# Kernel optimization log

Measured on AMD Instinct MI355X. Metric: run time of the kernel, lower is better.

The kernel has to match this reference:

```python
import jax, jax.numpy as jnp
import numpy as np
from jax import lax

B = 128; LEADS = 12; T = 1000; DM = 128; DI = 256; DS = 16; DR = 8; DC = 4; NB = 4; L = 199; OUT = 256


def _ln(x, g, b):
    m = x.mean(-1, keepdims=True)
    v = ((x - m) ** 2).mean(-1, keepdims=True)
    return (x - m) * lax.rsqrt(v + 1e-5) * g + b


def _ssm_scan(u, delta, A, Bm, Cm, D):
    """Selective scan. u, delta: [B,L,DI]; Bm, Cm: [B,L,DS]; A: [DI,DS]; D: [DI]."""
    def step(h, inp):
        d_t, B_t, C_t, u_t = inp  # [B,DI],[B,DS],[B,DS],[B,DI]
        dA = jnp.exp(d_t[:, :, None] * A[None])            # [B,DI,DS]
        h = dA * h + (d_t * u_t)[:, :, None] * B_t[:, None, :]
        y = jnp.einsum('bds,bs->bd', h, C_t)
        return h, y
    h0 = jnp.zeros((u.shape[0], A.shape[0], A.shape[1]), u.dtype)
    xs = (jnp.moveaxis(delta, 1, 0), jnp.moveaxis(Bm, 1, 0),
          jnp.moveaxis(Cm, 1, 0), jnp.moveaxis(u, 1, 0))
    _, ys = lax.scan(step, h0, xs)
    return jnp.moveaxis(ys, 0, 1) + u * D[None, None, :]


def setup_inputs() -> dict:
    key = jax.random.key(0)
    ks = jax.random.split(key, 16)
    n = lambda k, shp, s: jax.random.normal(k, shp, jnp.float32) * s
    inp = {}
    inp['x'] = jax.random.normal(ks[0], (B, LEADS, T), jnp.float32)
    inp['pe_w'] = n(ks[1], (DM, LEADS, 10), 0.1)
    inp['pe_b'] = jnp.zeros((DM,), jnp.float32)
    inp['gn_g'] = jnp.ones((DM,), jnp.float32)
    inp['gn_b'] = jnp.zeros((DM,), jnp.float32)
    inp['pos'] = n(ks[2], (1, L, DM), 0.02)
    inp['ln1_g'] = jnp.ones((NB, DM), jnp.float32)
    inp['ln1_b'] = jnp.zeros((NB, DM), jnp.float32)
    inp['in_w'] = n(ks[3], (NB, 2 * DI, DM), 0.05)
    inp['conv_w'] = n(ks[4], (NB, DI, DC), 0.2)
    inp['conv_b'] = jnp.zeros((NB, DI), jnp.float32)
    inp['xproj_w'] = n(ks[5], (NB, DR + 2 * DS, DI), 0.05)
    inp['dtproj_w'] = n(ks[6], (NB, DI, DR), 0.2)
    inp['dtproj_b'] = jnp.full((NB, DI), -4.6, jnp.float32)  # softplus(-4.6) ~= 0.01
    inp['A_log'] = jnp.tile(jnp.log(jnp.arange(1, DS + 1, dtype=jnp.float32))[None, None, :], (NB, DI, 1))
    inp['Dp'] = jnp.ones((NB, DI), jnp.float32)
    inp['outw'] = n(ks[7], (NB, DM, DI), 0.05)
    inp['ln2_g'] = jnp.ones((NB, DM), jnp.float32)
    inp['ln2_b'] = jnp.zeros((NB, DM), jnp.float32)
    inp['ffn_w1'] = n(ks[8], (NB, 4 * DM, DM), 0.05)
    inp['ffn_b1'] = jnp.zeros((NB, 4 * DM), jnp.float32)
    inp['ffn_w2'] = n(ks[9], (NB, DM, 4 * DM), 0.05)
    inp['ffn_b2'] = jnp.zeros((NB, DM), jnp.float32)
    inp['lnf_g'] = jnp.ones((DM,), jnp.float32)
    inp['lnf_b'] = jnp.zeros((DM,), jnp.float32)
    inp['head_w'] = n(ks[10], (OUT, DM), 0.05)
    inp['head_b'] = jnp.zeros((OUT,), jnp.float32)
    return inp


def reference(x, pe_w, pe_b, gn_g, gn_b, pos, ln1_g, ln1_b, in_w, conv_w, conv_b,
              xproj_w, dtproj_w, dtproj_b, A_log, Dp, outw, ln2_g, ln2_b,
              ffn_w1, ffn_b1, ffn_w2, ffn_b2, lnf_g, lnf_b, head_w, head_b):
    # --- patch embed: Conv1d(12 -> DM, k=10, s=5) + GroupNorm(8) + GELU ---
    h = lax.conv_general_dilated(x, pe_w, (5,), 'VALID',
                                 dimension_numbers=('NCH', 'OIH', 'NCH'))
    h = h + pe_b[None, :, None]                      # [B, DM, L]
    Bb, _, Lc = h.shape
    hg = h.reshape(Bb, 8, DM // 8, Lc)
    m = hg.mean((2, 3), keepdims=True)
    v = ((hg - m) ** 2).mean((2, 3), keepdims=True)
    h = ((hg - m) * lax.rsqrt(v + 1e-5)).reshape(Bb, DM, Lc)
    h = h * gn_g[None, :, None] + gn_b[None, :, None]
    h = jax.nn.gelu(h, approximate=False)
    h = jnp.swapaxes(h, 1, 2) + pos                  # [B, L, DM]

    for i in range(NB):
        # --- Mamba block ---
        u = _ln(h, ln1_g[i], ln1_b[i])
        xz = u @ in_w[i].T                           # [B, L, 2*DI]
        xm, z = jnp.split(xz, 2, axis=-1)
        xc = jnp.swapaxes(xm, 1, 2)                  # [B, DI, L]
        xc = jnp.pad(xc, ((0, 0), (0, 0), (DC - 1, 0)))  # causal pad
        xc = lax.conv_general_dilated(xc, conv_w[i][:, None, :], (1,), 'VALID',
                                      dimension_numbers=('NCH', 'OIH', 'NCH'),
                                      feature_group_count=DI)
        xc = xc + conv_b[i][None, :, None]
        u_ssm = jax.nn.silu(jnp.swapaxes(xc, 1, 2))  # [B, L, DI]
        dbl = u_ssm @ xproj_w[i].T                   # [B, L, DR+2*DS]
        dt, Bm, Cm = dbl[..., :DR], dbl[..., DR:DR + DS], dbl[..., DR + DS:]
        delta = jax.nn.softplus(dt @ dtproj_w[i].T + dtproj_b[i])  # [B, L, DI]
        A = -jnp.exp(A_log[i])                       # [DI, DS]
        y = _ssm_scan(u_ssm, delta, A, Bm, Cm, Dp[i])
        y = y * jax.nn.silu(z)
        h = h + y @ outw[i].T
        # --- FFN block ---
        f = _ln(h, ln2_g[i], ln2_b[i])
        f = jax.nn.gelu(f @ ffn_w1[i].T + ffn_b1[i], approximate=False)
        h = h + f @ ffn_w2[i].T + ffn_b2[i]

    h = _ln(h, lnf_g, lnf_b).mean(axis=1)            # [B, DM]
    return jax.nn.gelu(h @ head_w.T + head_b, approximate=False)  # [B, OUT]
```

## Files before the change

kernel.cpp:

```cpp
#include <hip/hip_runtime.h>
#include <math.h>

#define TOKS (128*199)
#define DM 128
#define DI 256
#define DS 16
#define DR 8
#define NBLK 4
#define LSEQ 199
#define BATCH 128

typedef __attribute__((ext_vector_type(8))) short bf16x8;
typedef __attribute__((ext_vector_type(4))) float f32x4;

__device__ __forceinline__ float gelu_f(float x) {
  return 0.5f * x * (1.0f + erff(x * 0.70710678118654752440f));
}
__device__ __forceinline__ float silu_f(float x) {
  return x / (1.0f + expf(-x));
}
__device__ __forceinline__ unsigned short f2bf(float f) {
  unsigned u = __float_as_uint(f);
  u += 0x7fffu + ((u >> 16) & 1u);
  return (unsigned short)(u >> 16);
}
__device__ __forceinline__ float bf2f(unsigned short h) {
  return __uint_as_float(((unsigned)h) << 16);
}

__global__ void pe_conv_kernel(const float* __restrict__ x, const float* __restrict__ pw,
                               const float* __restrict__ pb, float* __restrict__ convo) {
  int b = blockIdx.x;
  __shared__ float sx[12000];
  for (int i = threadIdx.x; i < 12000; i += 256) sx[i] = x[(size_t)b*12000 + i];
  __syncthreads();
  for (int o = threadIdx.x; o < DM*LSEQ; o += 256) {
    int m = o / LSEQ, t = o - m*LSEQ;
    const float* wr = pw + m*120;
    const float* xt = sx + t*5;
    float acc = pb[m];
#pragma unroll
    for (int l = 0; l < 12; ++l) {
#pragma unroll
      for (int k = 0; k < 10; ++k)
        acc += xt[l*1000 + k] * wr[l*10 + k];
    }
    convo[((size_t)b*DM + m)*LSEQ + t] = acc;
  }
}

__global__ void gn_kernel(const float* __restrict__ conv, const float* __restrict__ gg,
                          const float* __restrict__ gb, const float* __restrict__ pos,
                          float* __restrict__ h) {
  int b = blockIdx.x >> 3, grp = blockIdx.x & 7;
  const float* cb = conv + ((size_t)b*DM + grp*16)*LSEQ;
  int tid = threadIdx.x;
  float s = 0.f, s2 = 0.f;
  for (int i = tid; i < 16*LSEQ; i += 256) { float v = cb[i]; s += v; s2 += v*v; }
#pragma unroll
  for (int m = 1; m < 64; m <<= 1) { s += __shfl_xor(s, m); s2 += __shfl_xor(s2, m); }
  __shared__ float red[8];
  int lane = tid & 63, wid = tid >> 6;
  if (lane == 0) { red[wid] = s; red[4+wid] = s2; }
  __syncthreads();
  float S  = red[0]+red[1]+red[2]+red[3];
  float S2 = red[4]+red[5]+red[6]+red[7];
  const float inv = 1.0f/(16.0f*LSEQ);
  float mean = S*inv;
  float var  = S2*inv - mean*mean;
  float rstd = rsqrtf(var + 1e-5f);
  for (int i = tid; i < 16*LSEQ; i += 256) {
    int mloc = i / LSEQ; int t = i - mloc*LSEQ;
    int m = grp*16 + mloc;
    float v = (cb[i] - mean)*rstd*gg[m] + gb[m];
    v = gelu_f(v);
    h[((size_t)b*LSEQ + t)*DM + m] = v + pos[t*DM + m];
  }
}

__global__ void ln_kernel(const float* __restrict__ x, const float* __restrict__ g,
                          const float* __restrict__ bb, float* __restrict__ o) {
  int tok = blockIdx.x*4 + (threadIdx.x >> 6);
  int lane = threadIdx.x & 63;
  const float* xr = x + (size_t)tok*DM;
  float v0 = xr[lane], v1 = xr[lane+64];
  float s = v0+v1, s2 = v0*v0+v1*v1;
#pragma unroll
  for (int m=1;m<64;m<<=1){ s += __shfl_xor(s,m); s2 += __shfl_xor(s2,m); }
  float mean = s*(1.f/DM);
  float var  = s2*(1.f/DM) - mean*mean;
  float rs = rsqrtf(var+1e-5f);
  float* orow = o + (size_t)tok*DM;
  orow[lane]    = (v0-mean)*rs*g[lane]+bb[lane];
  orow[lane+64] = (v1-mean)*rs*g[lane+64]+bb[lane+64];
}

__device__ __forceinline__ void cvt_store(unsigned short* hp, unsigned short* lp,
                                          float4 x0, float4 x1) {
  float v[8] = {x0.x,x0.y,x0.z,x0.w,x1.x,x1.y,x1.z,x1.w};
  unsigned hi[4], lo[4];
#pragma unroll
  for (int j = 0; j < 4; ++j) {
    unsigned short h0 = f2bf(v[2*j]),   h1 = f2bf(v[2*j+1]);
    float r0 = v[2*j]   - bf2f(h0);
    float r1 = v[2*j+1] - bf2f(h1);
    unsigned short l0 = f2bf(r0), l1 = f2bf(r1);
    hi[j] = (unsigned)h0 | ((unsigned)h1 << 16);
    lo[j] = (unsigned)l0 | ((unsigned)l1 << 16);
  }
  *(uint4*)hp = make_uint4(hi[0],hi[1],hi[2],hi[3]);
  *(uint4*)lp = make_uint4(lo[0],lo[1],lo[2],lo[3]);
}

template<int ACT, int RESID, int BIAS, int WGUARD>
__global__ __launch_bounds__(256) void gemm_mfma(
    const float* __restrict__ A, const float* __restrict__ W,
    const float* __restrict__ bias, float* __restrict__ C,
    int N, int K, int Nw) {
  __shared__ unsigned short Ah[64][40], Al[64][40], Wh[64][40], Wl[64][40];
  int tid = threadIdx.x;
  int w = tid >> 6, l = tid & 63;
  int fr = l & 15, fq = l >> 4;
  int r = tid >> 2, seg = tid & 3;
  const float* Ap = A + (size_t)blockIdx.x*64*K + (size_t)r*K + seg*8;
  const float* Wp = W + (size_t)blockIdx.y*64*K + (size_t)r*K + seg*8;
  int wrow = blockIdx.y*64 + r;
  f32x4 acc[4];
#pragma unroll
  for (int ns = 0; ns < 4; ++ns) acc[ns] = (f32x4){0.f,0.f,0.f,0.f};

  for (int k0 = 0; k0 < K; k0 += 32) {
    float4 a0 = *(const float4*)(Ap + k0);
    float4 a1 = *(const float4*)(Ap + k0 + 4);
    float4 w0, w1;
    if (!WGUARD || wrow < Nw) {
      w0 = *(const float4*)(Wp + k0);
      w1 = *(const float4*)(Wp + k0 + 4);
    } else {
      w0 = make_float4(0.f,0.f,0.f,0.f); w1 = w0;
    }
    __syncthreads();
    cvt_store(&Ah[r][seg*8], &Al[r][seg*8], a0, a1);
    cvt_store(&Wh[r][seg*8], &Wl[r][seg*8], w0, w1);
    __syncthreads();
    bf16x8 ah = *(const bf16x8*)&Ah[w*16 + fr][fq*8];
    bf16x8 al = *(const bf16x8*)&Al[w*16 + fr][fq*8];
#pragma unroll
    for (int ns = 0; ns < 4; ++ns) {
      bf16x8 wh = *(const bf16x8*)&Wh[ns*16 + fr][fq*8];
      bf16x8 wl = *(const bf16x8*)&Wl[ns*16 + fr][fq*8];
      acc[ns] = __builtin_amdgcn_mfma_f32_16x16x32_bf16(ah, wh, acc[ns], 0, 0, 0);
      acc[ns] = __builtin_amdgcn_mfma_f32_16x16x32_bf16(al, wh, acc[ns], 0, 0, 0);
      acc[ns] = __builtin_amdgcn_mfma_f32_16x16x32_bf16(ah, wl, acc[ns], 0, 0, 0);
    }
  }
  int row0 = blockIdx.x*64 + w*16 + fq*4;
#pragma unroll
  for (int ns = 0; ns < 4; ++ns) {
    int col = blockIdx.y*64 + ns*16 + fr;
    if (WGUARD && col >= Nw) continue;
#pragma unroll
    for (int v = 0; v < 4; ++v) {
      float val = acc[ns][v];
      if (BIAS) val += bias[col];
      if (ACT)  val = gelu_f(val);
      float* cp = C + (size_t)(row0+v)*N + col;
      if (RESID) val += *cp;
      *cp = val;
    }
  }
}

__global__ void dwconv_kernel(const float* __restrict__ xz, const float* __restrict__ w,
                              const float* __restrict__ bias, float* __restrict__ uss) {
  int tok = blockIdx.x;
  int d = threadIdx.x;
  int b = tok / LSEQ, t = tok - b*LSEQ;
  float4 wv = *(const float4*)(w + d*4);
  float acc = bias[d];
  const float* xp = xz + ((size_t)b*LSEQ)*512 + d;
  if (t >= 3) acc += xp[(size_t)(t-3)*512]*wv.x;
  if (t >= 2) acc += xp[(size_t)(t-2)*512]*wv.y;
  if (t >= 1) acc += xp[(size_t)(t-1)*512]*wv.z;
  acc += xp[(size_t)t*512]*wv.w;
  uss[(size_t)tok*DI + d] = silu_f(acc);
}

__global__ __launch_bounds__(256) void dtproj_kernel(
    const float* __restrict__ dbl, const float* __restrict__ dtw,
    const float* __restrict__ dtb, float* __restrict__ dlt) {
  int tok = blockIdx.x;
  int d = threadIdx.x;
  __shared__ float sdt[8];
  if (d < 8) sdt[d] = dbl[(size_t)tok*40 + d];
  __syncthreads();
  float acc = dtb[d];
#pragma unroll
  for (int rr = 0; rr < DR; ++rr) acc += sdt[rr]*dtw[d*DR + rr];
  acc = (acc > 20.f) ? acc : log1pf(expf(acc));
  dlt[(size_t)tok*DI + d] = acc;
}

__global__ __launch_bounds__(256) void scan_kernel(
    const float* __restrict__ uss, float* __restrict__ dlt_y,
    const float* __restrict__ dbl,
    const float* __restrict__ A_log, const float* __restrict__ Dp,
    const float* __restrict__ xz) {
  int bg = blockIdx.x;
  int b = bg >> 4, dg = bg & 15;
  int tid = threadIdx.x;
  int s = tid & 15, dloc = tid >> 4;
  int d = dg*16 + dloc;
  float As = -expf(A_log[d*DS + s]);
  float Dd = Dp[d];
  float h = 0.f;
  size_t tokbase = (size_t)b*LSEQ;
  const float* pdt = dlt_y + tokbase*DI + d;
  const float* pu  = uss   + tokbase*DI + d;
  const float* pz  = xz    + tokbase*512 + 256 + d;
  const float* pB  = dbl   + tokbase*40 + 8  + s;
  const float* pC  = dbl   + tokbase*40 + 24 + s;
  float* po = dlt_y + tokbase*DI + d;
  float dt_c = *pdt, u_c = *pu, z_c = *pz, B_c = *pB, C_c = *pC;
  for (int t = 0; t < LSEQ; ++t) {
    float dt = dt_c, u = u_c, z = z_c, Bv = B_c, Cv = C_c;
    if (t + 1 < LSEQ) {
      pdt += DI; pu += DI; pz += 512; pB += 40; pC += 40;
      dt_c = *pdt; u_c = *pu; z_c = *pz; B_c = *pB; C_c = *pC;
    }
    float dA = expf(dt*As);
    h = fmaf(dA, h, dt*u*Bv);
    float p = h*Cv;
    p += __shfl_xor(p, 1);
    p += __shfl_xor(p, 2);
    p += __shfl_xor(p, 4);
    p += __shfl_xor(p, 8);
    float yv = (p + u*Dd) * silu_f(z);
    if (s == 0) *po = yv;
    po += DI;
  }
}

__global__ void final_kernel(const float* __restrict__ h, const float* __restrict__ g,
                             const float* __restrict__ bta, const float* __restrict__ hw,
                             const float* __restrict__ hb, float* __restrict__ out) {
  int b = blockIdx.x;
  int tid = threadIdx.x, lane = tid & 63, wid = tid >> 6;
  float s0 = 0.f, s1 = 0.f;
  for (int t = wid; t < LSEQ; t += 4) {
    const float* hr = h + ((size_t)b*LSEQ + t)*DM;
    float v0 = hr[lane], v1 = hr[lane+64];
    float ss = v0+v1, ss2 = v0*v0+v1*v1;
#pragma unroll
    for (int m=1;m<64;m<<=1){ ss += __shfl_xor(ss,m); ss2 += __shfl_xor(ss2,m); }
    float mean = ss*(1.f/DM);
    float var  = ss2*(1.f/DM)-mean*mean;
    float rs = rsqrtf(var+1e-5f);
    s0 += (v0-mean)*rs*g[lane]+bta[lane];
    s1 += (v1-mean)*rs*g[lane+64]+bta[lane+64];
  }
  __shared__ float sm[4][128];
  sm[wid][lane] = s0; sm[wid][lane+64] = s1;
  __syncthreads();
  __shared__ float mv[128];
  if (tid < 128) mv[tid] = (sm[0][tid]+sm[1][tid]+sm[2][tid]+sm[3][tid]) * (1.f/199.f);
  __syncthreads();
  int j = tid;
  const float* wr = hw + (size_t)j*DM;
  float acc = hb[j];
#pragma unroll 4
  for (int k=0;k<DM;k++) acc += mv[k]*wr[k];
  out[(size_t)b*256 + j] = gelu_f(acc);
}

extern "C" void kernel_launch(void* const* d_in, const int* in_sizes, int n_in,
                              void* d_out, int out_size, void* d_ws, size_t ws_size,
                              hipStream_t stream) {
  const float* x       = (const float*)d_in[0];
  const float* pe_w    = (const float*)d_in[1];
  const float* pe_b    = (const float*)d_in[2];
  const float* gn_g    = (const float*)d_in[3];
  const float* gn_b    = (const float*)d_in[4];
  const float* pos     = (const float*)d_in[5];
  const float* ln1_g   = (const float*)d_in[6];
  const float* ln1_b   = (const float*)d_in[7];
  const float* in_w    = (const float*)d_in[8];
  const float* conv_w  = (const float*)d_in[9];
  const float* conv_b  = (const float*)d_in[10];
  const float* xproj_w = (const float*)d_in[11];
  const float* dtproj_w= (const float*)d_in[12];
  const float* dtproj_b= (const float*)d_in[13];
  const float* A_log   = (const float*)d_in[14];
  const float* Dp      = (const float*)d_in[15];
  const float* outw    = (const float*)d_in[16];
  const float* ln2_g   = (const float*)d_in[17];
  const float* ln2_b   = (const float*)d_in[18];
  const float* ffn_w1  = (const float*)d_in[19];
  const float* ffn_b1  = (const float*)d_in[20];
  const float* ffn_w2  = (const float*)d_in[21];
  const float* ffn_b2  = (const float*)d_in[22];
  const float* lnf_g   = (const float*)d_in[23];
  const float* lnf_b   = (const float*)d_in[24];
  const float* head_w  = (const float*)d_in[25];
  const float* head_b  = (const float*)d_in[26];
  float* out = (float*)d_out;

  float* ws  = (float*)d_ws;
  float* h   = ws;
  float* u   = h   + (size_t)TOKS*DM;
  float* xz  = u   + (size_t)TOKS*DM;
  float* uss = xz  + (size_t)TOKS*512;
  float* dlt = uss + (size_t)TOKS*DI;
  float* dbl = dlt + (size_t)TOKS*DI;

  pe_conv_kernel<<<BATCH, 256, 0, stream>>>(x, pe_w, pe_b, xz);
  gn_kernel<<<BATCH*8, 256, 0, stream>>>(xz, gn_g, gn_b, pos, h);

  for (int i = 0; i < NBLK; ++i) {
    ln_kernel<<<TOKS/4, 256, 0, stream>>>(h, ln1_g + i*DM, ln1_b + i*DM, u);
    gemm_mfma<0,0,0,0><<<dim3(TOKS/64, 8), 256, 0, stream>>>(
        u, in_w + (size_t)i*512*DM, nullptr, xz, 512, DM, 0);
    dwconv_kernel<<<TOKS, 256, 0, stream>>>(xz, conv_w + i*DI*4, conv_b + i*DI, uss);
    gemm_mfma<0,0,0,1><<<dim3(TOKS/64, 1), 256, 0, stream>>>(
        uss, xproj_w + (size_t)i*40*DI, nullptr, dbl, 40, DI, 40);
    dtproj_kernel<<<TOKS, 256, 0, stream>>>(
        dbl, dtproj_w + (size_t)i*DI*DR, dtproj_b + i*DI, dlt);
    scan_kernel<<<BATCH*16, 256, 0, stream>>>(
        uss, dlt, dbl, A_log + (size_t)i*DI*DS, Dp + i*DI, xz);
    gemm_mfma<0,1,0,0><<<dim3(TOKS/64, 2), 256, 0, stream>>>(
        dlt, outw + (size_t)i*DM*DI, nullptr, h, DM, DI, 0);
    ln_kernel<<<TOKS/4, 256, 0, stream>>>(h, ln2_g + i*DM, ln2_b + i*DM, u);
    gemm_mfma<1,0,1,0><<<dim3(TOKS/64, 8), 256, 0, stream>>>(
        u, ffn_w1 + (size_t)i*512*DM, ffn_b1 + i*512, xz, 512, DM, 0);
    gemm_mfma<0,1,1,0><<<dim3(TOKS/64, 2), 256, 0, stream>>>(
        xz, ffn_w2 + (size_t)i*DM*512, ffn_b2 + i*DM, h, DM, 512, 0);
  }

  final_kernel<<<BATCH, 256, 0, stream>>>(h, lnf_g, lnf_b, head_w, head_b, out);
}
```

Measured before the change: 1.629 ms.

## Split patch-embed conv over time chunks, batch dtproj tokens, use fast exp/silu

The patch-embedding conv now launches one block per (batch, 25-timestep chunk) and stages only the needed input window in shared memory. This raises parallelism from 128 blocks and reduces LDS use per block. dtproj handles 8 tokens per block with weights held in registers, which cuts launch count and repeated weight loads. The scan, dwconv and silu paths switch to fast __expf and hardware reciprocal, trading a little accuracy for fewer instructions.

```diff
diff --git a/kernel.cpp b/kernel.cpp
--- a/kernel.cpp
+++ b/kernel.cpp
@@ -16,8 +16,9 @@
 __device__ __forceinline__ float gelu_f(float x) {
   return 0.5f * x * (1.0f + erff(x * 0.70710678118654752440f));
 }
-__device__ __forceinline__ float silu_f(float x) {
-  return x / (1.0f + expf(-x));
+__device__ __forceinline__ float silu_fast(float x) {
+  float e = __expf(-x);
+  return x * __builtin_amdgcn_rcpf(1.0f + e);
 }
 __device__ __forceinline__ unsigned short f2bf(float f) {
   unsigned u = __float_as_uint(f);
@@ -28,24 +29,31 @@
   return __uint_as_float(((unsigned)h) << 16);
 }
 
-__global__ void pe_conv_kernel(const float* __restrict__ x, const float* __restrict__ pw,
-                               const float* __restrict__ pb, float* __restrict__ convo) {
-  int b = blockIdx.x;
-  __shared__ float sx[12000];
-  for (int i = threadIdx.x; i < 12000; i += 256) sx[i] = x[(size_t)b*12000 + i];
-  __syncthreads();
-  for (int o = threadIdx.x; o < DM*LSEQ; o += 256) {
-    int m = o / LSEQ, t = o - m*LSEQ;
+__global__ __launch_bounds__(256) void pe_conv_kernel(
+    const float* __restrict__ x, const float* __restrict__ pw,
+    const float* __restrict__ pb, float* __restrict__ convo) {
+  int b = blockIdx.x, tc = blockIdx.y;
+  int t0 = tc * 25;
+  int nt = (LSEQ - t0 < 25) ? (LSEQ - t0) : 25;
+  __shared__ float sx[12][136];
+  int tid = threadIdx.x;
+  for (int i = tid; i < 12*136; i += 256) {
+    int l = i / 136, k = i - l*136;
+    int idx = t0*5 + k;
+    sx[l][k] = (idx < 1000) ? x[(size_t)b*12000 + l*1000 + idx] : 0.f;
+  }
+  __syncthreads();
+  for (int o = tid; o < DM*nt; o += 256) {
+    int m = o / nt, tt = o - m*nt;
     const float* wr = pw + m*120;
-    const float* xt = sx + t*5;
     float acc = pb[m];
 #pragma unroll
     for (int l = 0; l < 12; ++l) {
 #pragma unroll
       for (int k = 0; k < 10; ++k)
-        acc += xt[l*1000 + k] * wr[l*10 + k];
-    }
-    convo[((size_t)b*DM + m)*LSEQ + t] = acc;
+        acc += sx[l][tt*5 + k] * wr[l*10 + k];
+    }
+    convo[((size_t)b*DM + m)*LSEQ + t0 + tt] = acc;
   }
 }
 
@@ -183,22 +191,29 @@
   if (t >= 2) acc += xp[(size_t)(t-2)*512]*wv.y;
   if (t >= 1) acc += xp[(size_t)(t-1)*512]*wv.z;
   acc += xp[(size_t)t*512]*wv.w;
-  uss[(size_t)tok*DI + d] = silu_f(acc);
+  uss[(size_t)tok*DI + d] = silu_fast(acc);
 }
 
 __global__ __launch_bounds__(256) void dtproj_kernel(
     const float* __restrict__ dbl, const float* __restrict__ dtw,
     const float* __restrict__ dtb, float* __restrict__ dlt) {
-  int tok = blockIdx.x;
+  int tok0 = blockIdx.x * 8;
   int d = threadIdx.x;
-  __shared__ float sdt[8];
-  if (d < 8) sdt[d] = dbl[(size_t)tok*40 + d];
-  __syncthreads();
-  float acc = dtb[d];
-#pragma unroll
-  for (int rr = 0; rr < DR; ++rr) acc += sdt[rr]*dtw[d*DR + rr];
-  acc = (acc > 20.f) ? acc : log1pf(expf(acc));
-  dlt[(size_t)tok*DI + d] = acc;
+  __shared__ float sdt[8][DR];
+  if (d < 64) sdt[d >> 3][d & 7] = dbl[(size_t)(tok0 + (d >> 3))*40 + (d & 7)];
+  float wreg[DR];
+#pragma unroll
+  for (int rr = 0; rr < DR; ++rr) wreg[rr] = dtw[d*DR + rr];
+  float b0 = dtb[d];
+  __syncthreads();
+#pragma unroll
+  for (int tt = 0; tt < 8; ++tt) {
+    float acc = b0;
+#pragma unroll
+    for (int rr = 0; rr < DR; ++rr) acc += sdt[tt][rr]*wreg[rr];
+    acc = (acc > 20.f) ? acc : log1pf(__expf(acc));
+    dlt[(size_t)(tok0 + tt)*DI + d] = acc;
+  }
 }
 
 __global__ __launch_bounds__(256) void scan_kernel(
@@ -211,7 +226,7 @@
   int tid = threadIdx.x;
   int s = tid & 15, dloc = tid >> 4;
   int d = dg*16 + dloc;
-  float As = -expf(A_log[d*DS + s]);
+  float As = -__expf(A_log[d*DS + s]);
   float Dd = Dp[d];
   float h = 0.f;
   size_t tokbase = (size_t)b*LSEQ;
@@ -228,14 +243,14 @@
       pdt += DI; pu += DI; pz += 512; pB += 40; pC += 40;
       dt_c = *pdt; u_c = *pu; z_c = *pz; B_c = *pB; C_c = *pC;
     }
-    float dA = expf(dt*As);
+    float dA = __expf(dt*As);
     h = fmaf(dA, h, dt*u*Bv);
     float p = h*Cv;
     p += __shfl_xor(p, 1);
     p += __shfl_xor(p, 2);
     p += __shfl_xor(p, 4);
     p += __shfl_xor(p, 8);
-    float yv = (p + u*Dd) * silu_f(z);
+    float yv = fmaf(u, Dd, p) * silu_fast(z);
     if (s == 0) *po = yv;
     po += DI;
   }
@@ -313,7 +328,7 @@
   float* dlt = uss + (size_t)TOKS*DI;
   float* dbl = dlt + (size_t)TOKS*DI;
 
-  pe_conv_kernel<<<BATCH, 256, 0, stream>>>(x, pe_w, pe_b, xz);
+  pe_conv_kernel<<<dim3(BATCH, 8), 256, 0, stream>>>(x, pe_w, pe_b, xz);
   gn_kernel<<<BATCH*8, 256, 0, stream>>>(xz, gn_g, gn_b, pos, h);
 
   for (int i = 0; i < NBLK; ++i) {
@@ -323,7 +338,7 @@
     dwconv_kernel<<<TOKS, 256, 0, stream>>>(xz, conv_w + i*DI*4, conv_b + i*DI, uss);
     gemm_mfma<0,0,0,1><<<dim3(TOKS/64, 1), 256, 0, stream>>>(
         uss, xproj_w + (size_t)i*40*DI, nullptr, dbl, 40, DI, 40);
-    dtproj_kernel<<<TOKS, 256, 0, stream>>>(
+    dtproj_kernel<<<TOKS/8, 256, 0, stream>>>(
         dbl, dtproj_w + (size_t)i*DI*DR, dtproj_b + i*DI, dlt);
     scan_kernel<<<BATCH*16, 256, 0, stream>>>(
         uss, dlt, dbl, A_log + (size_t)i*DI*DS, Dp + i*DI, xz);
```

New measurement: 1.353 ms. 1.2x faster.
